# Performance work log

Measured on AMD Instinct MI355X. Metric: run time of the kernel, lower is better.

Reference implementation:

```python
import jax, jax.numpy as jnp
import numpy as np
import math

N = 100000   # nodes
E = 1600000  # edges
D = 128      # embed_dim
H = 8        # nhead
HD = D // H  # head dim
EPS = 1e-16  # matches torch_geometric-style segment softmax eps


def _xavier(key, shape):
    fan_out, fan_in = shape
    lim = math.sqrt(6.0 / (fan_in + fan_out))
    return jax.random.uniform(key, shape, jnp.float32, -lim, lim)


def setup_inputs() -> dict:
    key = jax.random.key(0)
    ks = jax.random.split(key, 8)
    return {
        "feats": jax.random.normal(ks[0], (N, D), jnp.float32),
        "edge_index": jax.random.randint(ks[1], (E, 2), 0, N, dtype=jnp.int64),
        "edge_attr": jax.random.normal(ks[2], (E, 1), jnp.float32),
        "Wq": _xavier(ks[3], (D, D)), "bq": jnp.zeros((D,), jnp.float32),
        "Wk": _xavier(ks[4], (D, D)), "bk": jnp.zeros((D,), jnp.float32),
        "Wv": _xavier(ks[5], (D, D)), "bv": jnp.zeros((D,), jnp.float32),
        "Wo": _xavier(ks[6], (D, D)), "bo": jnp.zeros((D,), jnp.float32),
    }


def reference(feats, edge_index, edge_attr, Wq, bq, Wk, bk, Wv, bv, Wo, bo):
    # feats: [N, D]; edge_index: [E, 2] with r=src, c=dst; edge_attr unused (mult_attr=0)
    n = feats.shape[0]
    q = (feats @ Wq.T + bq).reshape(n, H, HD)  # [N, H, hd]
    k = (feats @ Wk.T + bk).reshape(n, H, HD)
    v = (feats @ Wv.T + bv).reshape(n, H, HD)

    r = edge_index[:, 0]
    c = edge_index[:, 1]

    # per-edge dot-product scores: q[dst] . k[src]
    scores = jnp.einsum('ehd,ehd->eh', q[c], k[r]) / math.sqrt(HD)  # [E, H]

    # segment softmax over edges grouped by destination node c
    smax = jax.ops.segment_max(scores, c, num_segments=n)  # [N, H]
    ex = jnp.exp(scores - smax[c])
    ssum = jax.ops.segment_sum(ex, c, num_segments=n)      # [N, H]
    alpha = ex / (ssum[c] + EPS)                           # [E, H]
    # (dropout is identity at eval time; mult_attr=0 so edge_attr unused)

    # weighted scatter-aggregate of values into destination nodes
    out = jax.ops.segment_sum(alpha[:, :, None] * v[r], c, num_segments=n)  # [N, H, hd]
    out = out.reshape(n, D) @ Wo.T + bo
    return out
```

## Files before the change

### kernel.cpp

```cpp
#include <hip/hip_runtime.h>
#include <hip/hip_bf16.h>

typedef __attribute__((ext_vector_type(8))) short bh8;
typedef __attribute__((ext_vector_type(4))) float f32x4;

__device__ __forceinline__ float bfbits2f(unsigned short s) {
    union { unsigned int u; float f; } cv;
    cv.u = ((unsigned int)s) << 16;
    return cv.f;
}
__device__ __forceinline__ unsigned short f2bfbits(float f) {
    union { float f; unsigned int u; } cv; cv.f = f;
    unsigned int u = cv.u;
    u += 0x7fffu + ((u >> 16) & 1u);
    return (unsigned short)(u >> 16);
}
__device__ __forceinline__ unsigned int pack2bf(float a, float b) {
    return (unsigned int)f2bfbits(a) | (((unsigned int)f2bfbits(b)) << 16);
}

__device__ __forceinline__ bh8 load_frag_f32(const float* __restrict__ p) {
    float4 f0 = *reinterpret_cast<const float4*>(p);
    float4 f1 = *reinterpret_cast<const float4*>(p + 4);
    bh8 r;
    r[0] = (short)f2bfbits(f0.x); r[1] = (short)f2bfbits(f0.y);
    r[2] = (short)f2bfbits(f0.z); r[3] = (short)f2bfbits(f0.w);
    r[4] = (short)f2bfbits(f1.x); r[5] = (short)f2bfbits(f1.y);
    r[6] = (short)f2bfbits(f1.z); r[7] = (short)f2bfbits(f1.w);
    return r;
}

__global__ __launch_bounds__(256)
void wconv_kernel(const float* __restrict__ w0, const float* __restrict__ w1,
                  const float* __restrict__ w2, const float* __restrict__ w3,
                  unsigned short* __restrict__ o0, unsigned short* __restrict__ o1,
                  unsigned short* __restrict__ o2, unsigned short* __restrict__ o3)
{
    const float* src[4] = {w0, w1, w2, w3};
    unsigned short* dst[4] = {o0, o1, o2, o3};
    const float* s = src[blockIdx.y];
    unsigned short* d = dst[blockIdx.y];
    int i = (blockIdx.x * 256 + threadIdx.x) * 4;
    float4 f = *reinterpret_cast<const float4*>(&s[i]);
    uint2 p;
    p.x = pack2bf(f.x, f.y);
    p.y = pack2bf(f.z, f.w);
    *reinterpret_cast<uint2*>(&d[i]) = p;
}

__global__ __launch_bounds__(256)
void qkv_scatter(const float* __restrict__ A,
                 const unsigned short* __restrict__ Wqb, const float* __restrict__ bq,
                 const unsigned short* __restrict__ Wkb, const float* __restrict__ bk,
                 const unsigned short* __restrict__ Wvb, const float* __restrict__ bv,
                 unsigned short* __restrict__ Oq, unsigned short* __restrict__ Ok,
                 unsigned short* __restrict__ Ov, int M, int gx,
                 const int* __restrict__ ei, const int* __restrict__ offsets,
                 const int* __restrict__ rank, int* __restrict__ sorted_r,
                 int E, int nsb)
{
    if (blockIdx.x >= (unsigned)gx) {
        int sb = blockIdx.x - gx;
        int stride = nsb * 256;
        for (int e = sb * 256 + threadIdx.x; e < E; e += stride) {
            int2 rc = reinterpret_cast<const int2*>(ei)[e];
            sorted_r[offsets[rc.y] + rank[e]] = rc.x;
        }
        return;
    }

    const int lane = threadIdx.x & 63;
    const int w    = threadIdx.x >> 6;
    const int r0   = blockIdx.x * 128 + w * 32;
    const int lr   = lane & 15;
    const int lk   = (lane >> 4) * 8;
    const int cq   = (lane >> 4) * 4;

    bh8 a[2][4];
    #pragma unroll
    for (int jt = 0; jt < 2; jt++) {
        int row = r0 + jt * 16 + lr; if (row >= M) row = M - 1;
        const float* ap = &A[(size_t)row * 128 + lk];
        #pragma unroll
        for (int ks = 0; ks < 4; ks++) a[jt][ks] = load_frag_f32(ap + ks * 32);
    }

    const unsigned short* Ws[3] = {Wqb, Wkb, Wvb};
    const float* Bs[3] = {bq, bk, bv};
    unsigned short* Os[3] = {Oq, Ok, Ov};

    #pragma unroll
    for (int wsel = 0; wsel < 3; wsel++) {
        const unsigned short* W = Ws[wsel];
        f32x4 acc[2][8];
        #pragma unroll
        for (int jt = 0; jt < 2; jt++)
            #pragma unroll
            for (int it = 0; it < 8; it++)
                #pragma unroll
                for (int q = 0; q < 4; q++) acc[jt][it][q] = 0.f;

        #pragma unroll
        for (int ks = 0; ks < 4; ks++) {
            bh8 b[8];
            #pragma unroll
            for (int it = 0; it < 8; it++)
                b[it] = *reinterpret_cast<const bh8*>(
                    &W[(size_t)(it * 16 + lr) * 128 + ks * 32 + lk]);
            #pragma unroll
            for (int jt = 0; jt < 2; jt++)
                #pragma unroll
                for (int it = 0; it < 8; it++)
                    acc[jt][it] = __builtin_amdgcn_mfma_f32_16x16x32_bf16(
                        b[it], a[jt][ks], acc[jt][it], 0, 0, 0);
        }

        const float* bias = Bs[wsel];
        unsigned short* O = Os[wsel];
        #pragma unroll
        for (int jt = 0; jt < 2; jt++) {
            int row = r0 + jt * 16 + lr;
            if (row >= M) continue;
            #pragma unroll
            for (int it = 0; it < 8; it++) {
                float4 b4 = *reinterpret_cast<const float4*>(&bias[it * 16 + cq]);
                uint2 pk;
                pk.x = pack2bf(acc[jt][it][0] + b4.x, acc[jt][it][1] + b4.y);
                pk.y = pack2bf(acc[jt][it][2] + b4.z, acc[jt][it][3] + b4.w);
                *reinterpret_cast<uint2*>(&O[(size_t)row * 128 + it * 16 + cq]) = pk;
            }
        }
    }
}

__global__ __launch_bounds__(256)
void out_gemm(const unsigned short* __restrict__ A, const unsigned short* __restrict__ Wb,
              const float* __restrict__ bias, float* __restrict__ O, int M)
{
    const int lane = threadIdx.x & 63;
    const int w    = threadIdx.x >> 6;
    const int r0   = blockIdx.x * 128 + w * 32;
    const int lr   = lane & 15;
    const int lk   = (lane >> 4) * 8;
    const int cq   = (lane >> 4) * 4;

    bh8 a[2][4];
    #pragma unroll
    for (int jt = 0; jt < 2; jt++) {
        int row = r0 + jt * 16 + lr; if (row >= M) row = M - 1;
        const unsigned short* ap = &A[(size_t)row * 128 + lk];
        #pragma unroll
        for (int ks = 0; ks < 4; ks++)
            a[jt][ks] = *reinterpret_cast<const bh8*>(ap + ks * 32);
    }

    f32x4 acc[2][8];
    #pragma unroll
    for (int jt = 0; jt < 2; jt++)
        #pragma unroll
        for (int it = 0; it < 8; it++)
            #pragma unroll
            for (int q = 0; q < 4; q++) acc[jt][it][q] = 0.f;

    #pragma unroll
    for (int ks = 0; ks < 4; ks++) {
        bh8 b[8];
        #pragma unroll
        for (int it = 0; it < 8; it++)
            b[it] = *reinterpret_cast<const bh8*>(
                &Wb[(size_t)(it * 16 + lr) * 128 + ks * 32 + lk]);
        #pragma unroll
        for (int jt = 0; jt < 2; jt++)
            #pragma unroll
            for (int it = 0; it < 8; it++)
                acc[jt][it] = __builtin_amdgcn_mfma_f32_16x16x32_bf16(
                    b[it], a[jt][ks], acc[jt][it], 0, 0, 0);
    }

    #pragma unroll
    for (int jt = 0; jt < 2; jt++) {
        int row = r0 + jt * 16 + lr;
        if (row >= M) continue;
        #pragma unroll
        for (int it = 0; it < 8; it++) {
            float4 b4 = *reinterpret_cast<const float4*>(&bias[it * 16 + cq]);
            float4 o;
            o.x = acc[jt][it][0] + b4.x;
            o.y = acc[jt][it][1] + b4.y;
            o.z = acc[jt][it][2] + b4.z;
            o.w = acc[jt][it][3] + b4.w;
            *reinterpret_cast<float4*>(&O[(size_t)row * 128 + it * 16 + cq]) = o;
        }
    }
}

__global__ void hist_kernel(const int* __restrict__ ei, int* __restrict__ counts,
                            int* __restrict__ rank, int E)
{
    int e = blockIdx.x * blockDim.x + threadIdx.x;
    if (e < E) {
        int2 rc = reinterpret_cast<const int2*>(ei)[e];
        rank[e] = atomicAdd(&counts[rc.y], 1);
    }
}

__device__ __forceinline__ int wave_incl_scan(int v, int lane) {
    #pragma unroll
    for (int off = 1; off < 64; off <<= 1) {
        int y = __shfl_up(v, off);
        if (lane >= off) v += y;
    }
    return v;
}

__global__ __launch_bounds__(1024)
void scan1_kernel(const int* __restrict__ counts, int* __restrict__ offs,
                  int* __restrict__ blkSum, int n)
{
    __shared__ int wsum[16];
    __shared__ int woff[16];
    const int t = threadIdx.x, lane = t & 63, w = t >> 6;
    int i = blockIdx.x * 1024 + t;
    int x = (i < n) ? counts[i] : 0;
    int v = wave_incl_scan(x, lane);
    if (lane == 63) wsum[w] = v;
    __syncthreads();
    if (t == 0) {
        int s = 0;
        #pragma unroll
        for (int j = 0; j < 16; j++) { int tmp = wsum[j]; woff[j] = s; s += tmp; }
        blkSum[blockIdx.x] = s;
    }
    __syncthreads();
    if (i < n) offs[i] = woff[w] + v - x;
}

__global__ void scan2_kernel(const int* __restrict__ blkSum, int* __restrict__ blkOff,
                             int* __restrict__ offs, int nb, int n)
{
    const int lane = threadIdx.x;
    int carry = 0;
    for (int base = 0; base < nb; base += 64) {
        int x = (base + lane < nb) ? blkSum[base + lane] : 0;
        int v = wave_incl_scan(x, lane);
        if (base + lane < nb) blkOff[base + lane] = carry + v - x;
        carry += __shfl(v, 63);
    }
    if (lane == 0) offs[n] = carry;
}

__global__ __launch_bounds__(1024)
void scan3_kernel(int* __restrict__ offs, const int* __restrict__ blkOff, int n)
{
    int i = blockIdx.x * 1024 + threadIdx.x;
    if (i < n) offs[i] += blkOff[blockIdx.x];
}

__global__ __launch_bounds__(256)
void edge_attn_kernel(const unsigned short* __restrict__ qb,
                      const unsigned short* __restrict__ kb,
                      const unsigned short* __restrict__ vb,
                      const int* __restrict__ offsets,
                      const int* __restrict__ sorted_r,
                      unsigned short* __restrict__ acc_out, int n)
{
    const int lane = threadIdx.x & 63;
    const int wid  = threadIdx.x >> 6;
    const int node = blockIdx.x * 4 + wid;
    if (node >= n) return;

    const int h    = lane & 7;
    const int eloc = lane >> 3;
    const int seg0 = __builtin_amdgcn_readfirstlane(offsets[node]);
    const int segL = __builtin_amdgcn_readfirstlane(offsets[node + 1]) - seg0;
    const int nch  = (segL + 7) >> 3;
    const int* __restrict__ sr = sorted_r + seg0;

    float qf[16];
    {
        const uint4* p = reinterpret_cast<const uint4*>(&qb[(size_t)node * 128 + h * 16]);
        uint4 u0 = p[0], u1 = p[1];
        unsigned int uu[8] = {u0.x, u0.y, u0.z, u0.w, u1.x, u1.y, u1.z, u1.w};
        #pragma unroll
        for (int i = 0; i < 8; i++) {
            qf[2 * i]     = bfbits2f((unsigned short)(uu[i] & 0xffffu));
            qf[2 * i + 1] = bfbits2f((unsigned short)(uu[i] >> 16));
        }
    }

    float acc0 = 0.f, acc1 = 0.f, ssum = 0.f;

    uint4 kA0, kA1, kB0, kB1;
    unsigned int vA[8], vB[8];

    if (nch > 0) {
        int idx = (eloc < segL) ? eloc : (segL - 1);
        int rk  = sr[idx];
        const uint4* kp = reinterpret_cast<const uint4*>(&kb[(size_t)rk * 128 + h * 16]);
        kA0 = kp[0]; kA1 = kp[1];
        int ec0 = (segL < 8) ? segL : 8;
        #pragma unroll
        for (int e = 0; e < 8; e++) {
            int re = sr[(e < ec0) ? e : (ec0 - 1)];
            vA[e] = *reinterpret_cast<const unsigned int*>(&vb[(size_t)re * 128 + 2 * lane]);
        }
    }

    auto step = [&](int c, const uint4& ck0, const uint4& ck1, const unsigned int (&cv)[8],
                    uint4& nk0, uint4& nk1, unsigned int (&nv)[8]) {
        const int base = c << 3;
        if (c + 1 < nch) {
            int nb   = base + 8;
            int nidx = nb + eloc;
            int rk   = sr[(nidx < segL) ? nidx : (segL - 1)];
            const uint4* kp = reinterpret_cast<const uint4*>(&kb[(size_t)rk * 128 + h * 16]);
            nk0 = kp[0]; nk1 = kp[1];
            int ecn = segL - nb; if (ecn > 8) ecn = 8;
            #pragma unroll
            for (int e = 0; e < 8; e++) {
                int re = sr[nb + ((e < ecn) ? e : (ecn - 1))];
                nv[e] = *reinterpret_cast<const unsigned int*>(&vb[(size_t)re * 128 + 2 * lane]);
            }
        }
        unsigned int uu[8] = {ck0.x, ck0.y, ck0.z, ck0.w, ck1.x, ck1.y, ck1.z, ck1.w};
        float s = 0.f;
        #pragma unroll
        for (int i = 0; i < 8; i++) {
            s += qf[2 * i]     * bfbits2f((unsigned short)(uu[i] & 0xffffu));
            s += qf[2 * i + 1] * bfbits2f((unsigned short)(uu[i] >> 16));
        }
        float ex = (base + eloc < segL) ? __expf(s * 0.25f) : 0.f;
        ssum += ex;
        #pragma unroll
        for (int e = 0; e < 8; e++) {
            float exv = __shfl(ex, e * 8 + eloc);
            acc0 += exv * bfbits2f((unsigned short)(cv[e] & 0xffffu));
            acc1 += exv * bfbits2f((unsigned short)(cv[e] >> 16));
        }
    };

    int c = 0;
    while (c < nch) {
        step(c, kA0, kA1, vA, kB0, kB1, vB); c++;
        if (c >= nch) break;
        step(c, kB0, kB1, vB, kA0, kA1, vA); c++;
    }

    ssum += __shfl_xor(ssum, 8);
    ssum += __shfl_xor(ssum, 16);
    ssum += __shfl_xor(ssum, 32);
    float den = __shfl(ssum, lane >> 3) + 1e-16f;
    float rd  = 1.0f / den;

    reinterpret_cast<unsigned int*>(acc_out)[(size_t)node * 64 + lane] =
        pack2bf(acc0 * rd, acc1 * rd);
}

extern "C" void kernel_launch(void* const* d_in, const int* in_sizes, int n_in,
                              void* d_out, int out_size, void* d_ws, size_t ws_size,
                              hipStream_t stream)
{
    const float* feats = (const float*)d_in[0];
    const int*   ei    = (const int*)d_in[1];
    const float* Wq = (const float*)d_in[3];
    const float* bq = (const float*)d_in[4];
    const float* Wk = (const float*)d_in[5];
    const float* bk = (const float*)d_in[6];
    const float* Wv = (const float*)d_in[7];
    const float* bv = (const float*)d_in[8];
    const float* Wo = (const float*)d_in[9];
    const float* bo = (const float*)d_in[10];
    float* out = (float*)d_out;

    const int N = in_sizes[0] / 128;
    const int E = in_sizes[1] / 2;
    const int nb = (N + 1023) / 1024;

    char* ws = (char*)d_ws;
    size_t off = 0;
    auto alloc = [&](size_t bytes) -> void* {
        void* p = ws + off;
        off += (bytes + 255) & ~(size_t)255;
        return p;
    };
    unsigned short* qb   = (unsigned short*)alloc((size_t)N * 128 * 2);
    unsigned short* kb   = (unsigned short*)alloc((size_t)N * 128 * 2);
    unsigned short* vb   = (unsigned short*)alloc((size_t)N * 128 * 2);
    unsigned short* accb = (unsigned short*)alloc((size_t)N * 128 * 2);
    int* rank     = (int*)accb;
    int* counts   = (int*)alloc(((size_t)N + 1) * 4);
    int* offsets  = (int*)alloc(((size_t)N + 1) * 4);
    int* sorted_r = (int*)alloc((size_t)E * 4);
    int* blkSum   = (int*)alloc(256 * 4);
    int* blkOff   = (int*)alloc(256 * 4);
    unsigned short* Wqb = (unsigned short*)alloc(128 * 128 * 2);
    unsigned short* Wkb = (unsigned short*)alloc(128 * 128 * 2);
    unsigned short* Wvb = (unsigned short*)alloc(128 * 128 * 2);
    unsigned short* Wob = (unsigned short*)alloc(128 * 128 * 2);

    hipMemsetAsync(counts, 0, ((size_t)N + 1) * 4, stream);

    wconv_kernel<<<dim3(16, 4), 256, 0, stream>>>(Wq, Wk, Wv, Wo, Wqb, Wkb, Wvb, Wob);

    hist_kernel<<<(E + 255) / 256, 256, 0, stream>>>(ei, counts, rank, E);
    scan1_kernel<<<nb, 1024, 0, stream>>>(counts, offsets, blkSum, N);
    scan2_kernel<<<1, 64, 0, stream>>>(blkSum, blkOff, offsets, nb, N);
    scan3_kernel<<<nb, 1024, 0, stream>>>(offsets, blkOff, N);

    const int gx  = (N + 127) / 128;
    const int nsb = 1024;
    qkv_scatter<<<gx + nsb, 256, 0, stream>>>(feats, Wqb, bq, Wkb, bk, Wvb, bv,
                                              qb, kb, vb, N, gx,
                                              ei, offsets, rank, sorted_r, E, nsb);

    edge_attn_kernel<<<(N + 3) / 4, 256, 0, stream>>>(qb, kb, vb, offsets, sorted_r, accb, N);

    out_gemm<<<gx, 256, 0, stream>>>(accb, Wob, bo, out, N);
}
```

Baseline: 302.6 us.

## Fuse weight conversion into histogram, pack edge records, partition scatter by destination range

Merges the weight bf16 conversion into the histogram kernel to save a launch. The histogram now writes a packed int2 record holding src, rank (in the upper bits) and dst, so the scatter reads one coalesced record instead of edge_index plus a separate rank array. The scatter blocks are split into 8 groups by destination-node range, and the scatter block count is doubled, so each group's offsets and sorted_r writes stay within a smaller region for better cache locality. In exchange every group rereads the full record array. The packing also assumes node ids fit in 17 bits and ranks fit in the remaining 15 bits.

```diff
diff --git a/kernel.cpp b/kernel.cpp
--- a/kernel.cpp
+++ b/kernel.cpp
@@ -31,176 +31,31 @@
 }
 
 __global__ __launch_bounds__(256)
-void wconv_kernel(const float* __restrict__ w0, const float* __restrict__ w1,
-                  const float* __restrict__ w2, const float* __restrict__ w3,
-                  unsigned short* __restrict__ o0, unsigned short* __restrict__ o1,
-                  unsigned short* __restrict__ o2, unsigned short* __restrict__ o3)
-{
-    const float* src[4] = {w0, w1, w2, w3};
-    unsigned short* dst[4] = {o0, o1, o2, o3};
-    const float* s = src[blockIdx.y];
-    unsigned short* d = dst[blockIdx.y];
-    int i = (blockIdx.x * 256 + threadIdx.x) * 4;
-    float4 f = *reinterpret_cast<const float4*>(&s[i]);
-    uint2 p;
-    p.x = pack2bf(f.x, f.y);
-    p.y = pack2bf(f.z, f.w);
-    *reinterpret_cast<uint2*>(&d[i]) = p;
-}
-
-__global__ __launch_bounds__(256)
-void qkv_scatter(const float* __restrict__ A,
-                 const unsigned short* __restrict__ Wqb, const float* __restrict__ bq,
-                 const unsigned short* __restrict__ Wkb, const float* __restrict__ bk,
-                 const unsigned short* __restrict__ Wvb, const float* __restrict__ bv,
-                 unsigned short* __restrict__ Oq, unsigned short* __restrict__ Ok,
-                 unsigned short* __restrict__ Ov, int M, int gx,
-                 const int* __restrict__ ei, const int* __restrict__ offsets,
-                 const int* __restrict__ rank, int* __restrict__ sorted_r,
-                 int E, int nsb)
-{
-    if (blockIdx.x >= (unsigned)gx) {
-        int sb = blockIdx.x - gx;
-        int stride = nsb * 256;
-        for (int e = sb * 256 + threadIdx.x; e < E; e += stride) {
-            int2 rc = reinterpret_cast<const int2*>(ei)[e];
-            sorted_r[offsets[rc.y] + rank[e]] = rc.x;
-        }
+void wconv_hist(const float* __restrict__ w0, const float* __restrict__ w1,
+                const float* __restrict__ w2, const float* __restrict__ w3,
+                unsigned short* __restrict__ o0, unsigned short* __restrict__ o1,
+                unsigned short* __restrict__ o2, unsigned short* __restrict__ o3,
+                const int* __restrict__ ei, int* __restrict__ counts,
+                int2* __restrict__ erec, int E)
+{
+    if (blockIdx.x < 64) {
+        const float* src[4] = {w0, w1, w2, w3};
+        unsigned short* dst[4] = {o0, o1, o2, o3};
+        const float* s = src[blockIdx.x >> 4];
+        unsigned short* d = dst[blockIdx.x >> 4];
+        int i = ((blockIdx.x & 15) * 256 + threadIdx.x) * 4;
+        float4 f = *reinterpret_cast<const float4*>(&s[i]);
+        uint2 p;
+        p.x = pack2bf(f.x, f.y);
+        p.y = pack2bf(f.z, f.w);
+        *reinterpret_cast<uint2*>(&d[i]) = p;
         return;
     }
-
-    const int lane = threadIdx.x & 63;
-    const int w    = threadIdx.x >> 6;
-    const int r0   = blockIdx.x * 128 + w * 32;
-    const int lr   = lane & 15;
-    const int lk   = (lane >> 4) * 8;
-    const int cq   = (lane >> 4) * 4;
-
-    bh8 a[2][4];
-    #pragma unroll
-    for (int jt = 0; jt < 2; jt++) {
-        int row = r0 + jt * 16 + lr; if (row >= M) row = M - 1;
-        const float* ap = &A[(size_t)row * 128 + lk];
-        #pragma unroll
-        for (int ks = 0; ks < 4; ks++) a[jt][ks] = load_frag_f32(ap + ks * 32);
-    }
-
-    const unsigned short* Ws[3] = {Wqb, Wkb, Wvb};
-    const float* Bs[3] = {bq, bk, bv};
-    unsigned short* Os[3] = {Oq, Ok, Ov};
-
-    #pragma unroll
-    for (int wsel = 0; wsel < 3; wsel++) {
-        const unsigned short* W = Ws[wsel];
-        f32x4 acc[2][8];
-        #pragma unroll
-        for (int jt = 0; jt < 2; jt++)
-            #pragma unroll
-            for (int it = 0; it < 8; it++)
-                #pragma unroll
-                for (int q = 0; q < 4; q++) acc[jt][it][q] = 0.f;
-
-        #pragma unroll
-        for (int ks = 0; ks < 4; ks++) {
-            bh8 b[8];
-            #pragma unroll
-            for (int it = 0; it < 8; it++)
-                b[it] = *reinterpret_cast<const bh8*>(
-                    &W[(size_t)(it * 16 + lr) * 128 + ks * 32 + lk]);
-            #pragma unroll
-            for (int jt = 0; jt < 2; jt++)
-                #pragma unroll
-                for (int it = 0; it < 8; it++)
-                    acc[jt][it] = __builtin_amdgcn_mfma_f32_16x16x32_bf16(
-                        b[it], a[jt][ks], acc[jt][it], 0, 0, 0);
-        }
-
-        const float* bias = Bs[wsel];
-        unsigned short* O = Os[wsel];
-        #pragma unroll
-        for (int jt = 0; jt < 2; jt++) {
-            int row = r0 + jt * 16 + lr;
-            if (row >= M) continue;
-            #pragma unroll
-            for (int it = 0; it < 8; it++) {
-                float4 b4 = *reinterpret_cast<const float4*>(&bias[it * 16 + cq]);
-                uint2 pk;
-                pk.x = pack2bf(acc[jt][it][0] + b4.x, acc[jt][it][1] + b4.y);
-                pk.y = pack2bf(acc[jt][it][2] + b4.z, acc[jt][it][3] + b4.w);
-                *reinterpret_cast<uint2*>(&O[(size_t)row * 128 + it * 16 + cq]) = pk;
-            }
-        }
-    }
-}
-
-__global__ __launch_bounds__(256)
-void out_gemm(const unsigned short* __restrict__ A, const unsigned short* __restrict__ Wb,
-              const float* __restrict__ bias, float* __restrict__ O, int M)
-{
-    const int lane = threadIdx.x & 63;
-    const int w    = threadIdx.x >> 6;
-    const int r0   = blockIdx.x * 128 + w * 32;
-    const int lr   = lane & 15;
-    const int lk   = (lane >> 4) * 8;
-    const int cq   = (lane >> 4) * 4;
-
-    bh8 a[2][4];
-    #pragma unroll
-    for (int jt = 0; jt < 2; jt++) {
-        int row = r0 + jt * 16 + lr; if (row >= M) row = M - 1;
-        const unsigned short* ap = &A[(size_t)row * 128 + lk];
-        #pragma unroll
-        for (int ks = 0; ks < 4; ks++)
-            a[jt][ks] = *reinterpret_cast<const bh8*>(ap + ks * 32);
-    }
-
-    f32x4 acc[2][8];
-    #pragma unroll
-    for (int jt = 0; jt < 2; jt++)
-        #pragma unroll
-        for (int it = 0; it < 8; it++)
-            #pragma unroll
-            for (int q = 0; q < 4; q++) acc[jt][it][q] = 0.f;
-
-    #pragma unroll
-    for (int ks = 0; ks < 4; ks++) {
-        bh8 b[8];
-        #pragma unroll
-        for (int it = 0; it < 8; it++)
-            b[it] = *reinterpret_cast<const bh8*>(
-                &Wb[(size_t)(it * 16 + lr) * 128 + ks * 32 + lk]);
-        #pragma unroll
-        for (int jt = 0; jt < 2; jt++)
-            #pragma unroll
-            for (int it = 0; it < 8; it++)
-                acc[jt][it] = __builtin_amdgcn_mfma_f32_16x16x32_bf16(
-                    b[it], a[jt][ks], acc[jt][it], 0, 0, 0);
-    }
-
-    #pragma unroll
-    for (int jt = 0; jt < 2; jt++) {
-        int row = r0 + jt * 16 + lr;
-        if (row >= M) continue;
-        #pragma unroll
-        for (int it = 0; it < 8; it++) {
-            float4 b4 = *reinterpret_cast<const float4*>(&bias[it * 16 + cq]);
-            float4 o;
-            o.x = acc[jt][it][0] + b4.x;
-            o.y = acc[jt][it][1] + b4.y;
-            o.z = acc[jt][it][2] + b4.z;
-            o.w = acc[jt][it][3] + b4.w;
-            *reinterpret_cast<float4*>(&O[(size_t)row * 128 + it * 16 + cq]) = o;
-        }
-    }
-}
-
-__global__ void hist_kernel(const int* __restrict__ ei, int* __restrict__ counts,
-                            int* __restrict__ rank, int E)
-{
-    int e = blockIdx.x * blockDim.x + threadIdx.x;
+    int e = (blockIdx.x - 64) * 256 + threadIdx.x;
     if (e < E) {
         int2 rc = reinterpret_cast<const int2*>(ei)[e];
-        rank[e] = atomicAdd(&counts[rc.y], 1);
+        unsigned int rk = (unsigned int)atomicAdd(&counts[rc.y], 1);
+        erec[e] = make_int2((int)((unsigned int)rc.x | (rk << 17)), rc.y);
     }
 }
 
@@ -257,6 +112,99 @@
 }
 
 __global__ __launch_bounds__(256)
+void qkv_scatter(const float* __restrict__ A,
+                 const unsigned short* __restrict__ Wqb, const float* __restrict__ bq,
+                 const unsigned short* __restrict__ Wkb, const float* __restrict__ bk,
+                 const unsigned short* __restrict__ Wvb, const float* __restrict__ bv,
+                 unsigned short* __restrict__ Oq, unsigned short* __restrict__ Ok,
+                 unsigned short* __restrict__ Ov, int M, int gx,
+                 const int2* __restrict__ erec, const int* __restrict__ offsets,
+                 int* __restrict__ sorted_r, int E, int nsb)
+{
+    if (blockIdx.x >= (unsigned)gx) {
+        const int grp  = blockIdx.x & 7;
+        const int j    = blockIdx.x - gx;
+        const int big  = j >> 3;
+        const int nbg  = nsb >> 3;
+        const int segN = (M + 7) >> 3;
+        const int lo   = grp * segN;
+        const int hi   = (lo + segN < M) ? (lo + segN) : M;
+        const int stride = nbg * 256;
+        for (int e = big * 256 + threadIdx.x; e < E; e += stride) {
+            int2 rec = erec[e];
+            if (rec.y >= lo && rec.y < hi) {
+                unsigned int rx = (unsigned int)rec.x;
+                sorted_r[offsets[rec.y] + (int)(rx >> 17)] = (int)(rx & 0x1FFFFu);
+            }
+        }
+        return;
+    }
+
+    const int lane = threadIdx.x & 63;
+    const int w    = threadIdx.x >> 6;
+    const int r0   = blockIdx.x * 128 + w * 32;
+    const int lr   = lane & 15;
+    const int lk   = (lane >> 4) * 8;
+    const int cq   = (lane >> 4) * 4;
+
+    bh8 a[2][4];
+    #pragma unroll
+    for (int jt = 0; jt < 2; jt++) {
+        int row = r0 + jt * 16 + lr; if (row >= M) row = M - 1;
+        const float* ap = &A[(size_t)row * 128 + lk];
+        #pragma unroll
+        for (int ks = 0; ks < 4; ks++) a[jt][ks] = load_frag_f32(ap + ks * 32);
+    }
+
+    const unsigned short* Ws[3] = {Wqb, Wkb, Wvb};
+    const float* Bs[3] = {bq, bk, bv};
+    unsigned short* Os[3] = {Oq, Ok, Ov};
+
+    #pragma unroll
+    for (int wsel = 0; wsel < 3; wsel++) {
+        const unsigned short* W = Ws[wsel];
+        f32x4 acc[2][8];
+        #pragma unroll
+        for (int jt = 0; jt < 2; jt++)
+            #pragma unroll
+            for (int it = 0; it < 8; it++)
+                #pragma unroll
+                for (int q = 0; q < 4; q++) acc[jt][it][q] = 0.f;
+
+        #pragma unroll
+        for (int ks = 0; ks < 4; ks++) {
+            bh8 b[8];
+            #pragma unroll
+            for (int it = 0; it < 8; it++)
+                b[it] = *reinterpret_cast<const bh8*>(
+                    &W[(size_t)(it * 16 + lr) * 128 + ks * 32 + lk]);
+            #pragma unroll
+            for (int jt = 0; jt < 2; jt++)
+                #pragma unroll
+                for (int it = 0; it < 8; it++)
+                    acc[jt][it] = __builtin_amdgcn_mfma_f32_16x16x32_bf16(
+                        b[it], a[jt][ks], acc[jt][it], 0, 0, 0);
+        }
+
+        const float* bias = Bs[wsel];
+        unsigned short* O = Os[wsel];
+        #pragma unroll
+        for (int jt = 0; jt < 2; jt++) {
+            int row = r0 + jt * 16 + lr;
+            if (row >= M) continue;
+            #pragma unroll
+            for (int it = 0; it < 8; it++) {
+                float4 b4 = *reinterpret_cast<const float4*>(&bias[it * 16 + cq]);
+                uint2 pk;
+                pk.x = pack2bf(acc[jt][it][0] + b4.x, acc[jt][it][1] + b4.y);
+                pk.y = pack2bf(acc[jt][it][2] + b4.z, acc[jt][it][3] + b4.w);
+                *reinterpret_cast<uint2*>(&O[(size_t)row * 128 + it * 16 + cq]) = pk;
+            }
+        }
+    }
+}
+
+__global__ __launch_bounds__(256)
 void edge_attn_kernel(const unsigned short* __restrict__ qb,
                       const unsigned short* __restrict__ kb,
                       const unsigned short* __restrict__ vb,
@@ -354,6 +302,67 @@
 
     reinterpret_cast<unsigned int*>(acc_out)[(size_t)node * 64 + lane] =
         pack2bf(acc0 * rd, acc1 * rd);
+}
+
+__global__ __launch_bounds__(256)
+void out_gemm(const unsigned short* __restrict__ A, const unsigned short* __restrict__ Wb,
+              const float* __restrict__ bias, float* __restrict__ O, int M)
+{
+    const int lane = threadIdx.x & 63;
+    const int w    = threadIdx.x >> 6;
+    const int r0   = blockIdx.x * 128 + w * 32;
+    const int lr   = lane & 15;
+    const int lk   = (lane >> 4) * 8;
+    const int cq   = (lane >> 4) * 4;
+
+    bh8 a[2][4];
+    #pragma unroll
+    for (int jt = 0; jt < 2; jt++) {
+        int row = r0 + jt * 16 + lr; if (row >= M) row = M - 1;
+        const unsigned short* ap = &A[(size_t)row * 128 + lk];
+        #pragma unroll
+        for (int ks = 0; ks < 4; ks++)
+            a[jt][ks] = *reinterpret_cast<const bh8*>(ap + ks * 32);
+    }
+
+    f32x4 acc[2][8];
+    #pragma unroll
+    for (int jt = 0; jt < 2; jt++)
+        #pragma unroll
+        for (int it = 0; it < 8; it++)
+            #pragma unroll
+            for (int q = 0; q < 4; q++) acc[jt][it][q] = 0.f;
+
+    #pragma unroll
+    for (int ks = 0; ks < 4; ks++) {
+        bh8 b[8];
+        #pragma unroll
+        for (int it = 0; it < 8; it++)
+            b[it] = *reinterpret_cast<const bh8*>(
+                &Wb[(size_t)(it * 16 + lr) * 128 + ks * 32 + lk]);
+        #pragma unroll
+        for (int jt = 0; jt < 2; jt++)
+            #pragma unroll
+            for (int it = 0; it < 8; it++)
+                acc[jt][it] = __builtin_amdgcn_mfma_f32_16x16x32_bf16(
+                    b[it], a[jt][ks], acc[jt][it], 0, 0, 0);
+    }
+
+    #pragma unroll
+    for (int jt = 0; jt < 2; jt++) {
+        int row = r0 + jt * 16 + lr;
+        if (row >= M) continue;
+        #pragma unroll
+        for (int it = 0; it < 8; it++) {
+            float4 b4 = *reinterpret_cast<const float4*>(&bias[it * 16 + cq]);
+            float4 o;
+            o.x = acc[jt][it][0] + b4.x;
+            o.y = acc[jt][it][1] + b4.y;
+            o.z = acc[jt][it][2] + b4.z;
+            o.w = acc[jt][it][3] + b4.w;
+            *reinterpret_cast<float4*>(&O[(size_t)row * 128 + it * 16 + cq]) = o;
+        }
+    }
 }
 
 extern "C" void kernel_launch(void* const* d_in, const int* in_sizes, int n_in,
@@ -387,7 +396,7 @@
     unsigned short* kb   = (unsigned short*)alloc((size_t)N * 128 * 2);
     unsigned short* vb   = (unsigned short*)alloc((size_t)N * 128 * 2);
     unsigned short* accb = (unsigned short*)alloc((size_t)N * 128 * 2);
-    int* rank     = (int*)accb;
+    int2* erec    = (int2*)accb;
     int* counts   = (int*)alloc(((size_t)N + 1) * 4);
     int* offsets  = (int*)alloc(((size_t)N + 1) * 4);
     int* sorted_r = (int*)alloc((size_t)E * 4);
@@ -400,18 +409,18 @@
 
     hipMemsetAsync(counts, 0, ((size_t)N + 1) * 4, stream);
 
-    wconv_kernel<<<dim3(16, 4), 256, 0, stream>>>(Wq, Wk, Wv, Wo, Wqb, Wkb, Wvb, Wob);
-
-    hist_kernel<<<(E + 255) / 256, 256, 0, stream>>>(ei, counts, rank, E);
+    wconv_hist<<<64 + (E + 255) / 256, 256, 0, stream>>>(
+        Wq, Wk, Wv, Wo, Wqb, Wkb, Wvb, Wob, ei, counts, erec, E);
+
     scan1_kernel<<<nb, 1024, 0, stream>>>(counts, offsets, blkSum, N);
     scan2_kernel<<<1, 64, 0, stream>>>(blkSum, blkOff, offsets, nb, N);
     scan3_kernel<<<nb, 1024, 0, stream>>>(offsets, blkOff, N);
 
     const int gx  = (N + 127) / 128;
-    const int nsb = 1024;
+    const int nsb = 2048;
     qkv_scatter<<<gx + nsb, 256, 0, stream>>>(feats, Wqb, bq, Wkb, bk, Wvb, bv,
                                               qb, kb, vb, N, gx,
-                                              ei, offsets, rank, sorted_r, E, nsb);
+                                              erec, offsets, sorted_r, E, nsb);
 
     edge_attn_kernel<<<(N + 3) / 4, 256, 0, stream>>>(qb, kb, vb, offsets, sorted_r, accb, N);
 
```

Measured after the change: 334.0 us. +10.4%, slower.

## Fuse output projection into edge attention and histogram into weight conversion

Applied to the files above, without the earlier changes.

Moves the Wo projection into the edge-attention kernel: each wave stages its normalized node output in shared memory and computes the 128x128 matvec with scalar FMAs against bf16 Wo, writing fp32 output directly. This removes the bf16 intermediate buffer round trip and the separate MFMA GEMM launch, at the cost of much more per-node ALU work and repeated Wo reads from cache. It also merges weight conversion with the edge histogram into one launch, uses nontemporal stores for the sorted source scatter, and doubles the scatter block count.

```diff
diff --git a/kernel.cpp b/kernel.cpp
--- a/kernel.cpp
+++ b/kernel.cpp
@@ -31,21 +31,83 @@
 }
 
 __global__ __launch_bounds__(256)
-void wconv_kernel(const float* __restrict__ w0, const float* __restrict__ w1,
-                  const float* __restrict__ w2, const float* __restrict__ w3,
-                  unsigned short* __restrict__ o0, unsigned short* __restrict__ o1,
-                  unsigned short* __restrict__ o2, unsigned short* __restrict__ o3)
-{
-    const float* src[4] = {w0, w1, w2, w3};
-    unsigned short* dst[4] = {o0, o1, o2, o3};
-    const float* s = src[blockIdx.y];
-    unsigned short* d = dst[blockIdx.y];
-    int i = (blockIdx.x * 256 + threadIdx.x) * 4;
-    float4 f = *reinterpret_cast<const float4*>(&s[i]);
-    uint2 p;
-    p.x = pack2bf(f.x, f.y);
-    p.y = pack2bf(f.z, f.w);
-    *reinterpret_cast<uint2*>(&d[i]) = p;
+void wconv_hist(const float* __restrict__ w0, const float* __restrict__ w1,
+                const float* __restrict__ w2, const float* __restrict__ w3,
+                unsigned short* __restrict__ o0, unsigned short* __restrict__ o1,
+                unsigned short* __restrict__ o2, unsigned short* __restrict__ o3,
+                const int* __restrict__ ei, int* __restrict__ counts,
+                int* __restrict__ rank, int E)
+{
+    if (blockIdx.x < 64) {
+        const float* src[4] = {w0, w1, w2, w3};
+        unsigned short* dst[4] = {o0, o1, o2, o3};
+        const float* s = src[blockIdx.x >> 4];
+        unsigned short* d = dst[blockIdx.x >> 4];
+        int i = ((blockIdx.x & 15) * 256 + threadIdx.x) * 4;
+        float4 f = *reinterpret_cast<const float4*>(&s[i]);
+        uint2 p;
+        p.x = pack2bf(f.x, f.y);
+        p.y = pack2bf(f.z, f.w);
+        *reinterpret_cast<uint2*>(&d[i]) = p;
+        return;
+    }
+    int e = (blockIdx.x - 64) * 256 + threadIdx.x;
+    if (e < E) {
+        int2 rc = reinterpret_cast<const int2*>(ei)[e];
+        rank[e] = atomicAdd(&counts[rc.y], 1);
+    }
+}
+
+__device__ __forceinline__ int wave_incl_scan(int v, int lane) {
+    #pragma unroll
+    for (int off = 1; off < 64; off <<= 1) {
+        int y = __shfl_up(v, off);
+        if (lane >= off) v += y;
+    }
+    return v;
+}
+
+__global__ __launch_bounds__(1024)
+void scan1_kernel(const int* __restrict__ counts, int* __restrict__ offs,
+                  int* __restrict__ blkSum, int n)
+{
+    __shared__ int wsum[16];
+    __shared__ int woff[16];
+    const int t = threadIdx.x, lane = t & 63, w = t >> 6;
+    int i = blockIdx.x * 1024 + t;
+    int x = (i < n) ? counts[i] : 0;
+    int v = wave_incl_scan(x, lane);
+    if (lane == 63) wsum[w] = v;
+    __syncthreads();
+    if (t == 0) {
+        int s = 0;
+        #pragma unroll
+        for (int j = 0; j < 16; j++) { int tmp = wsum[j]; woff[j] = s; s += tmp; }
+        blkSum[blockIdx.x] = s;
+    }
+    __syncthreads();
+    if (i < n) offs[i] = woff[w] + v - x;
+}
+
+__global__ void scan2_kernel(const int* __restrict__ blkSum, int* __restrict__ blkOff,
+                             int* __restrict__ offs, int nb, int n)
+{
+    const int lane = threadIdx.x;
+    int carry = 0;
+    for (int base = 0; base < nb; base += 64) {
+        int x = (base + lane < nb) ? blkSum[base + lane] : 0;
+        int v = wave_incl_scan(x, lane);
+        if (base + lane < nb) blkOff[base + lane] = carry + v - x;
+        carry += __shfl(v, 63);
+    }
+    if (lane == 0) offs[n] = carry;
+}
+
+__global__ __launch_bounds__(1024)
+void scan3_kernel(int* __restrict__ offs, const int* __restrict__ blkOff, int n)
+{
+    int i = blockIdx.x * 1024 + threadIdx.x;
+    if (i < n) offs[i] += blkOff[blockIdx.x];
 }
 
 __global__ __launch_bounds__(256)
@@ -64,7 +126,7 @@
         int stride = nsb * 256;
         for (int e = sb * 256 + threadIdx.x; e < E; e += stride) {
             int2 rc = reinterpret_cast<const int2*>(ei)[e];
-            sorted_r[offsets[rc.y] + rank[e]] = rc.x;
+            __builtin_nontemporal_store(rc.x, &sorted_r[offsets[rc.y] + rank[e]]);
         }
         return;
     }
@@ -134,151 +196,32 @@
 }
 
 __global__ __launch_bounds__(256)
-void out_gemm(const unsigned short* __restrict__ A, const unsigned short* __restrict__ Wb,
-              const float* __restrict__ bias, float* __restrict__ O, int M)
-{
-    const int lane = threadIdx.x & 63;
-    const int w    = threadIdx.x >> 6;
-    const int r0   = blockIdx.x * 128 + w * 32;
-    const int lr   = lane & 15;
-    const int lk   = (lane >> 4) * 8;
-    const int cq   = (lane >> 4) * 4;
-
-    bh8 a[2][4];
-    #pragma unroll
-    for (int jt = 0; jt < 2; jt++) {
-        int row = r0 + jt * 16 + lr; if (row >= M) row = M - 1;
-        const unsigned short* ap = &A[(size_t)row * 128 + lk];
-        #pragma unroll
-        for (int ks = 0; ks < 4; ks++)
-            a[jt][ks] = *reinterpret_cast<const bh8*>(ap + ks * 32);
-    }
-
-    f32x4 acc[2][8];
-    #pragma unroll
-    for (int jt = 0; jt < 2; jt++)
-        #pragma unroll
-        for (int it = 0; it < 8; it++)
-            #pragma unroll
-            for (int q = 0; q < 4; q++) acc[jt][it][q] = 0.f;
-
-    #pragma unroll
-    for (int ks = 0; ks < 4; ks++) {
-        bh8 b[8];
-        #pragma unroll
-        for (int it = 0; it < 8; it++)
-            b[it] = *reinterpret_cast<const bh8*>(
-                &Wb[(size_t)(it * 16 + lr) * 128 + ks * 32 + lk]);
-        #pragma unroll
-        for (int jt = 0; jt < 2; jt++)
-            #pragma unroll
-            for (int it = 0; it < 8; it++)
-                acc[jt][it] = __builtin_amdgcn_mfma_f32_16x16x32_bf16(
-                    b[it], a[jt][ks], acc[jt][it], 0, 0, 0);
-    }
-
-    #pragma unroll
-    for (int jt = 0; jt < 2; jt++) {
-        int row = r0 + jt * 16 + lr;
-        if (row >= M) continue;
-        #pragma unroll
-        for (int it = 0; it < 8; it++) {
-            float4 b4 = *reinterpret_cast<const float4*>(&bias[it * 16 + cq]);
-            float4 o;
-            o.x = acc[jt][it][0] + b4.x;
-            o.y = acc[jt][it][1] + b4.y;
-            o.z = acc[jt][it][2] + b4.z;
-            o.w = acc[jt][it][3] + b4.w;
-            *reinterpret_cast<float4*>(&O[(size_t)row * 128 + it * 16 + cq]) = o;
-        }
-    }
-}
-
-__global__ void hist_kernel(const int* __restrict__ ei, int* __restrict__ counts,
-                            int* __restrict__ rank, int E)
-{
-    int e = blockIdx.x * blockDim.x + threadIdx.x;
-    if (e < E) {
-        int2 rc = reinterpret_cast<const int2*>(ei)[e];
-        rank[e] = atomicAdd(&counts[rc.y], 1);
-    }
-}
-
-__device__ __forceinline__ int wave_incl_scan(int v, int lane) {
-    #pragma unroll
-    for (int off = 1; off < 64; off <<= 1) {
-        int y = __shfl_up(v, off);
-        if (lane >= off) v += y;
-    }
-    return v;
-}
-
-__global__ __launch_bounds__(1024)
-void scan1_kernel(const int* __restrict__ counts, int* __restrict__ offs,
-                  int* __restrict__ blkSum, int n)
-{
-    __shared__ int wsum[16];
-    __shared__ int woff[16];
-    const int t = threadIdx.x, lane = t & 63, w = t >> 6;
-    int i = blockIdx.x * 1024 + t;
-    int x = (i < n) ? counts[i] : 0;
-    int v = wave_incl_scan(x, lane);
-    if (lane == 63) wsum[w] = v;
-    __syncthreads();
-    if (t == 0) {
-        int s = 0;
-        #pragma unroll
-        for (int j = 0; j < 16; j++) { int tmp = wsum[j]; woff[j] = s; s += tmp; }
-        blkSum[blockIdx.x] = s;
-    }
-    __syncthreads();
-    if (i < n) offs[i] = woff[w] + v - x;
-}
-
-__global__ void scan2_kernel(const int* __restrict__ blkSum, int* __restrict__ blkOff,
-                             int* __restrict__ offs, int nb, int n)
-{
-    const int lane = threadIdx.x;
-    int carry = 0;
-    for (int base = 0; base < nb; base += 64) {
-        int x = (base + lane < nb) ? blkSum[base + lane] : 0;
-        int v = wave_incl_scan(x, lane);
-        if (base + lane < nb) blkOff[base + lane] = carry + v - x;
-        carry += __shfl(v, 63);
-    }
-    if (lane == 0) offs[n] = carry;
-}
-
-__global__ __launch_bounds__(1024)
-void scan3_kernel(int* __restrict__ offs, const int* __restrict__ blkOff, int n)
-{
-    int i = blockIdx.x * 1024 + threadIdx.x;
-    if (i < n) offs[i] += blkOff[blockIdx.x];
-}
-
-__global__ __launch_bounds__(256)
 void edge_attn_kernel(const unsigned short* __restrict__ qb,
                       const unsigned short* __restrict__ kb,
                       const unsigned short* __restrict__ vb,
                       const int* __restrict__ offsets,
                       const int* __restrict__ sorted_r,
-                      unsigned short* __restrict__ acc_out, int n)
-{
+                      const unsigned short* __restrict__ Wob,
+                      const float* __restrict__ bo,
+                      float* __restrict__ out, int n)
+{
+    __shared__ float olds[4][128];
+
     const int lane = threadIdx.x & 63;
     const int wid  = threadIdx.x >> 6;
     const int node = blockIdx.x * 4 + wid;
-    if (node >= n) return;
+    const int nodeC = (node < n) ? node : (n - 1);
 
     const int h    = lane & 7;
     const int eloc = lane >> 3;
-    const int seg0 = __builtin_amdgcn_readfirstlane(offsets[node]);
-    const int segL = __builtin_amdgcn_readfirstlane(offsets[node + 1]) - seg0;
+    const int seg0 = __builtin_amdgcn_readfirstlane(offsets[nodeC]);
+    const int segL = __builtin_amdgcn_readfirstlane(offsets[nodeC + 1]) - seg0;
     const int nch  = (segL + 7) >> 3;
     const int* __restrict__ sr = sorted_r + seg0;
 
     float qf[16];
     {
-        const uint4* p = reinterpret_cast<const uint4*>(&qb[(size_t)node * 128 + h * 16]);
+        const uint4* p = reinterpret_cast<const uint4*>(&qb[(size_t)nodeC * 128 + h * 16]);
         uint4 u0 = p[0], u1 = p[1];
         unsigned int uu[8] = {u0.x, u0.y, u0.z, u0.w, u1.x, u1.y, u1.z, u1.w};
         #pragma unroll
@@ -352,8 +295,31 @@
     float den = __shfl(ssum, lane >> 3) + 1e-16f;
     float rd  = 1.0f / den;
 
-    reinterpret_cast<unsigned int*>(acc_out)[(size_t)node * 64 + lane] =
-        pack2bf(acc0 * rd, acc1 * rd);
+    olds[wid][2 * lane]     = acc0 * rd;
+    olds[wid][2 * lane + 1] = acc1 * rd;
+    __syncthreads();
+
+    const unsigned short* wr0 = &Wob[(size_t)(2 * lane) * 128];
+    const unsigned short* wr1 = wr0 + 128;
+    float s0 = 0.f, s1 = 0.f;
+    #pragma unroll
+    for (int kc = 0; kc < 16; kc++) {
+        bh8 w0 = *reinterpret_cast<const bh8*>(wr0 + kc * 8);
+        bh8 w1 = *reinterpret_cast<const bh8*>(wr1 + kc * 8);
+        #pragma unroll
+        for (int j = 0; j < 8; j++) {
+            float of = olds[wid][kc * 8 + j];
+            s0 += of * bfbits2f((unsigned short)w0[j]);
+            s1 += of * bfbits2f((unsigned short)w1[j]);
+        }
+    }
+    if (node < n) {
+        float2 ob = *reinterpret_cast<const float2*>(&bo[2 * lane]);
+        float2 r;
+        r.x = s0 + ob.x;
+        r.y = s1 + ob.y;
+        *reinterpret_cast<float2*>(&out[(size_t)node * 128 + 2 * lane]) = r;
+    }
 }
 
 extern "C" void kernel_launch(void* const* d_in, const int* in_sizes, int n_in,
@@ -386,8 +352,7 @@
     unsigned short* qb   = (unsigned short*)alloc((size_t)N * 128 * 2);
     unsigned short* kb   = (unsigned short*)alloc((size_t)N * 128 * 2);
     unsigned short* vb   = (unsigned short*)alloc((size_t)N * 128 * 2);
-    unsigned short* accb = (unsigned short*)alloc((size_t)N * 128 * 2);
-    int* rank     = (int*)accb;
+    int* rank     = (int*)alloc((size_t)N * 128 * 2);
     int* counts   = (int*)alloc(((size_t)N + 1) * 4);
     int* offsets  = (int*)alloc(((size_t)N + 1) * 4);
     int* sorted_r = (int*)alloc((size_t)E * 4);
@@ -400,20 +365,19 @@
 
     hipMemsetAsync(counts, 0, ((size_t)N + 1) * 4, stream);
 
-    wconv_kernel<<<dim3(16, 4), 256, 0, stream>>>(Wq, Wk, Wv, Wo, Wqb, Wkb, Wvb, Wob);
-
-    hist_kernel<<<(E + 255) / 256, 256, 0, stream>>>(ei, counts, rank, E);
+    wconv_hist<<<64 + (E + 255) / 256, 256, 0, stream>>>(
+        Wq, Wk, Wv, Wo, Wqb, Wkb, Wvb, Wob, ei, counts, rank, E);
+
     scan1_kernel<<<nb, 1024, 0, stream>>>(counts, offsets, blkSum, N);
     scan2_kernel<<<1, 64, 0, stream>>>(blkSum, blkOff, offsets, nb, N);
     scan3_kernel<<<nb, 1024, 0, stream>>>(offsets, blkOff, N);
 
     const int gx  = (N + 127) / 128;
-    const int nsb = 1024;
+    const int nsb = 2048;
     qkv_scatter<<<gx + nsb, 256, 0, stream>>>(feats, Wqb, bq, Wkb, bk, Wvb, bv,
                                               qb, kb, vb, N, gx,
                                               ei, offsets, rank, sorted_r, E, nsb);
 
-    edge_attn_kernel<<<(N + 3) / 4, 256, 0, stream>>>(qb, kb, vb, offsets, sorted_r, accb, N);
-
-    out_gemm<<<gx, 256, 0, stream>>>(accb, Wob, bo, out, N);
-}
+    edge_attn_kernel<<<(N + 3) / 4, 256, 0, stream>>>(
+        qb, kb, vb, offsets, sorted_r, Wob, bo, out, N);
+}
```

Measured after the change: 601.4 us. 1.99x slower.
